# Kernel tuning notes

Hardware: AMD Instinct MI355X
Metric: run time of the kernel (lower is better)

## Reference

```python
import jax, jax.numpy as jnp
import numpy as np

B, L, DIM = 2, 2048, 2048
N_HEADS, N_KV_HEADS = 32, 8
HEAD_DIM = DIM // N_HEADS  # 64
SCALE = HEAD_DIM ** -0.5


def setup_inputs() -> dict:
    key = jax.random.key(0)
    ks = jax.random.split(key, 6)
    s = 0.02
    x = jax.random.normal(ks[0], (B, L, DIM), dtype=jnp.float32)
    wq = jax.random.normal(ks[1], (N_HEADS * HEAD_DIM, DIM), dtype=jnp.float32) * s
    wk = jax.random.normal(ks[2], (N_KV_HEADS * HEAD_DIM, DIM), dtype=jnp.float32) * s
    wv = jax.random.normal(ks[3], (N_KV_HEADS * HEAD_DIM, DIM), dtype=jnp.float32) * s
    wo = jax.random.normal(ks[4], (DIM, N_HEADS * HEAD_DIM), dtype=jnp.float32) * s
    # standard RoPE frequencies: theta = 10000^(-2i/d), angle = pos * theta
    inv_freq = 1.0 / (10000.0 ** (jnp.arange(0, HEAD_DIM, 2, dtype=jnp.float32) / HEAD_DIM))
    angles = jnp.arange(L, dtype=jnp.float32)[:, None] * inv_freq[None, :]  # [L, HEAD_DIM//2]
    freqs_cos = jnp.cos(angles)
    freqs_sin = jnp.sin(angles)
    # additive causal mask [1, 1, L, L]
    causal = jnp.tril(jnp.ones((L, L), dtype=bool))
    mask = jnp.where(causal, 0.0, -1e9).astype(jnp.float32)[None, None]
    return {"x": x, "wq": wq, "wk": wk, "wv": wv, "wo": wo,
            "freqs_cos": freqs_cos, "freqs_sin": freqs_sin, "mask": mask}


def _apply_rope(t, cos, sin):
    # t: [B, H, L, D]; complex pairing is (even, odd) interleaved along D
    te, to = t[..., 0::2], t[..., 1::2]
    cos = cos[None, None, : t.shape[2], :]
    sin = sin[None, None, : t.shape[2], :]
    re = te * cos - to * sin
    im = te * sin + to * cos
    return jnp.stack([re, im], axis=-1).reshape(t.shape)


def reference(x, wq, wk, wv, wo, freqs_cos, freqs_sin, mask):
    b, l, _ = x.shape
    q = (x @ wq.T).reshape(b, l, N_HEADS, HEAD_DIM).transpose(0, 2, 1, 3)
    k = (x @ wk.T).reshape(b, l, N_KV_HEADS, HEAD_DIM).transpose(0, 2, 1, 3)
    v = (x @ wv.T).reshape(b, l, N_KV_HEADS, HEAD_DIM).transpose(0, 2, 1, 3)
    q = _apply_rope(q, freqs_cos, freqs_sin)
    k = _apply_rope(k, freqs_cos, freqs_sin)
    repeats = N_HEADS // N_KV_HEADS
    k = jnp.repeat(k, repeats, axis=1)
    v = jnp.repeat(v, repeats, axis=1)
    scores = jnp.einsum("bhqd,bhkd->bhqk", q, k) * SCALE + mask
    probs = jax.nn.softmax(scores, axis=-1)
    out = jnp.einsum("bhqk,bhkd->bhqd", probs, v)
    out = out.transpose(0, 2, 1, 3).reshape(b, l, N_HEADS * HEAD_DIM)
    return out @ wo.T
```

## Files before the change

### kernel.cpp

```cpp
#include <hip/hip_runtime.h>
#include <hip/hip_bf16.h>
#include <stdint.h>

typedef __attribute__((ext_vector_type(8))) short bf16x8;
typedef __attribute__((ext_vector_type(4))) float f32x4;
typedef __attribute__((ext_vector_type(16))) float f32x16;
typedef __attribute__((ext_vector_type(4))) unsigned int u32x4;

#define B_    2
#define L_    2048
#define DIM_  2048
#define NH_   32
#define NKV_  8
#define HD_   64
#define KVD_  512
#define CLOG_ 0.1803368801111244f

__device__ __forceinline__ unsigned short f2bf(float f) {
  unsigned u = __float_as_uint(f);
  u += 0x7fff + ((u >> 16) & 1);
  return (unsigned short)(u >> 16);
}
__device__ __forceinline__ unsigned cvtpk(float lo, float hi_) {
  unsigned r;
  asm("v_cvt_pk_bf16_f32 %0, %1, %2" : "=v"(r) : "v"(lo), "v"(hi_));
  return r;
}
__device__ __forceinline__ float bf2f(unsigned short h) {
  return __uint_as_float(((unsigned)h) << 16);
}

#define GLDS16(gsrc, ldst) __builtin_amdgcn_global_load_lds( \
    (const __attribute__((address_space(1))) unsigned int*)(gsrc), \
    (__attribute__((address_space(3))) unsigned int*)(ldst), 16, 0, 0)

__global__ void cvt_all(const float* __restrict__ x,  const float* __restrict__ wq,
                        const float* __restrict__ wk, const float* __restrict__ wv,
                        const float* __restrict__ wo,
                        unsigned short* __restrict__ xb,  unsigned short* __restrict__ wqb,
                        unsigned short* __restrict__ wkb, unsigned short* __restrict__ wvb,
                        unsigned short* __restrict__ wob) {
  int i = blockIdx.x * blockDim.x + threadIdx.x;
  const float* src; unsigned short* dst; int off;
  if (i < 2097152)      { src = x;  dst = xb;  off = i; }
  else if (i < 3145728) { src = wq; dst = wqb; off = i - 2097152; }
  else if (i < 3407872) { src = wk; dst = wkb; off = i - 3145728; }
  else if (i < 3670016) { src = wv; dst = wvb; off = i - 3407872; }
  else                  { src = wo; dst = wob; off = i - 3670016; }
  float4 v = reinterpret_cast<const float4*>(src)[off];
  ushort4 o;
  o.x = f2bf(v.x); o.y = f2bf(v.y); o.z = f2bf(v.z); o.w = f2bf(v.w);
  reinterpret_cast<ushort4*>(dst)[off] = o;
}

template<int OUTMODE>
__device__ __forceinline__ void gemm128_core(
    const unsigned short* __restrict__ A,
    const unsigned short* __restrict__ W,
    void* __restrict__ C, int N, int K, int m0, int n0,
    unsigned short (*As)[128 * 64], unsigned short (*Bs)[128 * 64])
{
  const int tid = threadIdx.x;
  const int lane = tid & 63, wid = tid >> 6;
  const int wm = wid >> 1, wn = wid & 1;
  const int r = lane & 15, g = lane >> 4;
  const int rsw = (r & 7) << 4;
  f32x4 acc[4][4] = {};

  auto STAGE = [&](int buf, int k0) {
#pragma unroll
    for (int p = 0; p < 4; ++p) {
      int off = (p * 256 + tid) * 16;
      int row = off >> 7;
      int colb = (off & 127) ^ ((row & 7) << 4);
      GLDS16((const char*)A + ((size_t)(m0 + row) * K + k0) * 2 + colb,
             (char*)As[buf] + off);
      GLDS16((const char*)W + ((size_t)(n0 + row) * K + k0) * 2 + colb,
             (char*)Bs[buf] + off);
    }
  };

  const int nt = K >> 6;
  STAGE(0, 0);
  asm volatile("s_waitcnt vmcnt(0)" ::: "memory");
  __builtin_amdgcn_s_barrier();
  int cur = 0;
  for (int kt = 0; kt < nt; ++kt) {
    if (kt + 1 < nt) {
      STAGE(cur ^ 1, (kt + 1) << 6);
      asm volatile("s_waitcnt vmcnt(8)" ::: "memory");
    } else {
      asm volatile("s_waitcnt vmcnt(0)" ::: "memory");
    }
    __builtin_amdgcn_s_barrier();
    __builtin_amdgcn_sched_barrier(0);
    const char* Ab = (const char*)As[cur];
    const char* Bb = (const char*)Bs[cur];
    __builtin_amdgcn_s_setprio(1);
#pragma unroll
    for (int kk = 0; kk < 2; ++kk) {
      bf16x8 af[4], bfv[4];
#pragma unroll
      for (int i = 0; i < 4; ++i)
        af[i] = *reinterpret_cast<const bf16x8*>(
            Ab + (wm * 64 + i * 16 + r) * 128 + ((kk * 64 + g * 16) ^ rsw));
#pragma unroll
      for (int i = 0; i < 4; ++i)
        bfv[i] = *reinterpret_cast<const bf16x8*>(
            Bb + (wn * 64 + i * 16 + r) * 128 + ((kk * 64 + g * 16) ^ rsw));
#pragma unroll
      for (int i = 0; i < 4; ++i)
#pragma unroll
        for (int j = 0; j < 4; ++j)
          acc[i][j] = __builtin_amdgcn_mfma_f32_16x16x32_bf16(af[i], bfv[j], acc[i][j], 0, 0, 0);
    }
    __builtin_amdgcn_s_setprio(0);
    asm volatile("s_waitcnt lgkmcnt(0)" ::: "memory");
    __builtin_amdgcn_s_barrier();
    cur ^= 1;
  }

  if (OUTMODE == 2) {
#pragma unroll
    for (int i = 0; i < 4; ++i)
#pragma unroll
      for (int jf = 0; jf < 4; ++jf) {
        int col = n0 + wn * 64 + jf * 16 + r;
        int kvi = col >> 6, d = col & 63;
        int tok = m0 + wm * 64 + i * 16 + g * 4;
        int bb = tok >> 11, tl = tok & (L_ - 1);
        uint2 u;
        u.x = cvtpk(acc[i][jf][0], acc[i][jf][1]);
        u.y = cvtpk(acc[i][jf][2], acc[i][jf][3]);
        *reinterpret_cast<uint2*>((unsigned short*)C +
            ((size_t)((bb * NKV_ + kvi) * HD_ + d)) * L_ + tl) = u;
      }
  } else {
#pragma unroll
    for (int i = 0; i < 4; ++i)
#pragma unroll
      for (int jf = 0; jf < 4; ++jf)
#pragma unroll
        for (int j = 0; j < 4; ++j) {
          size_t row = (size_t)(m0 + wm * 64 + i * 16 + g * 4 + j);
          size_t col = (size_t)(n0 + wn * 64 + jf * 16 + r);
          float v = acc[i][jf][j];
          if (OUTMODE == 1) ((float*)C)[row * N + col] = v;
          else ((unsigned short*)C)[row * N + col] = f2bf(v);
        }
  }
}

template<int OUT_F32>
__global__ __launch_bounds__(256) void gemm_bt(
    const unsigned short* __restrict__ A,
    const unsigned short* __restrict__ W,
    void* __restrict__ C, int M, int N, int K)
{
  __shared__ unsigned short As[2][128 * 64];
  __shared__ unsigned short Bs[2][128 * 64];
  gemm128_core<OUT_F32 ? 1 : 0>(A, W, C, N, K, blockIdx.y * 128, blockIdx.x * 128, As, Bs);
}

__global__ __launch_bounds__(256) void gemm_qkv(
    const unsigned short* __restrict__ A,
    const unsigned short* __restrict__ Wq,
    const unsigned short* __restrict__ Wk,
    const unsigned short* __restrict__ Wv,
    unsigned short* __restrict__ Cq,
    unsigned short* __restrict__ Ck,
    unsigned short* __restrict__ Vt)
{
  __shared__ unsigned short As[2][128 * 64];
  __shared__ unsigned short Bs[2][128 * 64];
  const int bx = blockIdx.x;
  const int m0 = blockIdx.y * 128;
  if (bx < 16)
    gemm128_core<0>(A, Wq, Cq, 2048, DIM_, m0, bx * 128, As, Bs);
  else if (bx < 20)
    gemm128_core<0>(A, Wk, Ck, 512, DIM_, m0, (bx - 16) * 128, As, Bs);
  else
    gemm128_core<2>(A, Wv, Vt, 512, DIM_, m0, (bx - 20) * 128, As, Bs);
}

__global__ void rope_v8(unsigned short* __restrict__ t,
                        const float* __restrict__ fc,
                        const float* __restrict__ fs,
                        int rowElems, int lshift, float scale) {
  int idx = blockIdx.x * blockDim.x + threadIdx.x;
  int row = idx >> lshift;
  if (row >= B_ * L_) return;
  int pos = (idx & ((1 << lshift) - 1)) << 3;
  int l = row & (L_ - 1);
  int i0 = (pos & 63) >> 1;
  unsigned short* p = t + (size_t)row * rowElems + pos;
  uint4 v = *reinterpret_cast<const uint4*>(p);
  float4 c4 = *reinterpret_cast<const float4*>(fc + l * 32 + i0);
  float4 s4 = *reinterpret_cast<const float4*>(fs + l * 32 + i0);
  float cc[4] = {c4.x * scale, c4.y * scale, c4.z * scale, c4.w * scale};
  float ss[4] = {s4.x * scale, s4.y * scale, s4.z * scale, s4.w * scale};
  unsigned wds[4] = {v.x, v.y, v.z, v.w};
  uint4 o;
  unsigned ow[4];
#pragma unroll
  for (int k = 0; k < 4; ++k) {
    float te = bf2f((unsigned short)(wds[k] & 0xffff));
    float to = bf2f((unsigned short)(wds[k] >> 16));
    ow[k] = cvtpk(te * cc[k] - to * ss[k], te * ss[k] + to * cc[k]);
  }
  o.x = ow[0]; o.y = ow[1]; o.z = ow[2]; o.w = ow[3];
  *reinterpret_cast<uint4*>(p) = o;
}

__global__ __launch_bounds__(256) void attn_kernel(
    const unsigned short* __restrict__ Q,
    const unsigned short* __restrict__ K,
    const unsigned short* __restrict__ Vt,
    unsigned short* __restrict__ AO)
{
  __shared__ unsigned short Ks[2][64 * 64];
  __shared__ unsigned short Vs[2][64 * 64];
  const int tid = threadIdx.x;
  const int lane = tid & 63, w = tid >> 6;
  const int ql = lane & 31;
  const int hi = lane >> 5;
  const int wid = blockIdx.x;
  const int j = wid >> 6;
  const int blk = j >> 2, pos = j & 3;
  const int base = 15 - 4 * blk;
  const int qt = (blk & 1) ? (base - 3 + pos) : (base - pos);
  const int bh = wid & 63;
  const int b = bh >> 5, h = bh & 31, kv = h >> 2;
  const int q0 = qt * 128;
  const int qw = q0 + w * 32;
  const int nkt = (q0 + 128) >> 6;

  bf16x8 qf[4];
  const unsigned short* qbase = Q + ((size_t)(b * L_ + qw + ql)) * DIM_ + h * HD_ + hi * 8;
#pragma unroll
  for (int dk = 0; dk < 4; ++dk)
    qf[dk] = *reinterpret_cast<const bf16x8*>(qbase + dk * 16);

  const unsigned short* Kg = K + (size_t)b * L_ * KVD_ + kv * HD_;
  const unsigned short* Vg = Vt + ((size_t)(b * NKV_ + kv)) * HD_ * L_;

  f32x16 oacc0 = {}, oacc1 = {};
  float lrow = 0.f;
  const int rsw = (ql & 7) << 4;

  auto STAGE = [&](int buf, int t) {
    const int k0 = t * 64;
#pragma unroll
    for (int p = 0; p < 2; ++p) {
      int off = (p * 256 + tid) * 16;
      int row = off >> 7;
      int colb = (off & 127) ^ ((row & 7) << 4);
      GLDS16((const char*)Kg + ((size_t)(k0 + row)) * (KVD_ * 2) + colb,
             (char*)Ks[buf] + off);
      GLDS16((const char*)Vg + ((size_t)row) * (L_ * 2) + (size_t)k0 * 2 + colb,
             (char*)Vs[buf] + off);
    }
  };

  int cur = 0;
  STAGE(0, 0);
  __syncthreads();

  for (int t = 0; t < nkt; ++t) {
    if (t + 1 < nkt) STAGE(cur ^ 1, t + 1);
    const int k0 = t * 64;
    if (k0 < qw + 32) {
      const char* Kl = (const char*)Ks[cur];
      const char* Vl = (const char*)Vs[cur];
      f32x16 s0 = {}, s1 = {};
      __builtin_amdgcn_s_setprio(1);
#pragma unroll
      for (int dk = 0; dk < 4; ++dk) {
        bf16x8 kf0 = *reinterpret_cast<const bf16x8*>(Kl + ql * 128 + ((dk * 32 + hi * 16) ^ rsw));
        bf16x8 kf1 = *reinterpret_cast<const bf16x8*>(Kl + (32 + ql) * 128 + ((dk * 32 + hi * 16) ^ rsw));
        s0 = __builtin_amdgcn_mfma_f32_32x32x16_bf16(kf0, qf[dk], s0, 0, 0, 0);
        s1 = __builtin_amdgcn_mfma_f32_32x32x16_bf16(kf1, qf[dk], s1, 0, 0, 0);
      }
      __builtin_amdgcn_s_setprio(0);
      float p[32];
      float ps = 0.f;
      if (k0 + 63 > qw) {
        int q = qw + ql;
#pragma unroll
        for (int i = 0; i < 32; ++i) {
          float sv = (i < 16) ? s0[i] : s1[i - 16];
          int kk = k0 + (i >> 4) * 32 + (i & 3) + 8 * ((i & 15) >> 2) + 4 * hi;
          float e = exp2f(sv);
          e = (kk > q) ? 0.f : e;
          p[i] = e; ps += e;
        }
      } else {
#pragma unroll
        for (int i = 0; i < 32; ++i) {
          float sv = (i < 16) ? s0[i] : s1[i - 16];
          p[i] = exp2f(sv); ps += p[i];
        }
      }
      ps += __shfl_xor(ps, 32);
      lrow += ps;
      bf16x8 pf[4];
#pragma unroll
      for (int s = 0; s < 4; ++s) {
        int bp = ((s >> 1) << 4) + ((s & 1) << 3);
        unsigned w0 = cvtpk(p[bp + 0], p[bp + 1]);
        unsigned w1 = cvtpk(p[bp + 2], p[bp + 3]);
        unsigned w2 = cvtpk(p[bp + 4], p[bp + 5]);
        unsigned w3 = cvtpk(p[bp + 6], p[bp + 7]);
        unsigned x0 = (unsigned)__shfl_xor((int)w0, 32);
        unsigned x1 = (unsigned)__shfl_xor((int)w1, 32);
        unsigned x2 = (unsigned)__shfl_xor((int)w2, 32);
        unsigned x3 = (unsigned)__shfl_xor((int)w3, 32);
        u32x4 fw;
        fw[0] = hi ? x2 : w0;
        fw[1] = hi ? x3 : w1;
        fw[2] = hi ? w2 : x0;
        fw[3] = hi ? w3 : x1;
        pf[s] = __builtin_bit_cast(bf16x8, fw);
      }
      __builtin_amdgcn_s_setprio(1);
#pragma unroll
      for (int s = 0; s < 4; ++s) {
        bf16x8 v0 = *reinterpret_cast<const bf16x8*>(Vl + ql * 128 + ((s * 32 + hi * 16) ^ rsw));
        bf16x8 v1 = *reinterpret_cast<const bf16x8*>(Vl + (32 + ql) * 128 + ((s * 32 + hi * 16) ^ rsw));
        oacc0 = __builtin_amdgcn_mfma_f32_32x32x16_bf16(v0, pf[s], oacc0, 0, 0, 0);
        oacc1 = __builtin_amdgcn_mfma_f32_32x32x16_bf16(v1, pf[s], oacc1, 0, 0, 0);
      }
      __builtin_amdgcn_s_setprio(0);
    }
    __syncthreads();
    cur ^= 1;
  }

  float inv = 1.f / lrow;
  unsigned short* obase = AO + ((size_t)(b * L_ + qw + ql)) * DIM_ + h * HD_;
#pragma unroll
  for (int g4 = 0; g4 < 4; ++g4) {
    uint2 u;
    u.x = cvtpk(oacc0[g4 * 4 + 0] * inv, oacc0[g4 * 4 + 1] * inv);
    u.y = cvtpk(oacc0[g4 * 4 + 2] * inv, oacc0[g4 * 4 + 3] * inv);
    *reinterpret_cast<uint2*>(obase + g4 * 8 + hi * 4) = u;
    uint2 v;
    v.x = cvtpk(oacc1[g4 * 4 + 0] * inv, oacc1[g4 * 4 + 1] * inv);
    v.y = cvtpk(oacc1[g4 * 4 + 2] * inv, oacc1[g4 * 4 + 3] * inv);
    *reinterpret_cast<uint2*>(obase + 32 + g4 * 8 + hi * 4) = v;
  }
}

extern "C" void kernel_launch(void* const* d_in, const int* in_sizes, int n_in,
                              void* d_out, int out_size, void* d_ws, size_t ws_size,
                              hipStream_t stream) {
  const float* x  = (const float*)d_in[0];
  const float* wq = (const float*)d_in[1];
  const float* wk = (const float*)d_in[2];
  const float* wv = (const float*)d_in[3];
  const float* wo = (const float*)d_in[4];
  const float* fc = (const float*)d_in[5];
  const float* fs = (const float*)d_in[6];
  float* out = (float*)d_out;

  unsigned short* ws  = (unsigned short*)d_ws;
  unsigned short* xb  = ws;
  unsigned short* wqb = xb  + 8388608;
  unsigned short* wkb = wqb + 4194304;
  unsigned short* wvb = wkb + 1048576;
  unsigned short* wob = wvb + 1048576;
  unsigned short* Qb  = wob + 4194304;
  unsigned short* Kb  = Qb  + 8388608;
  unsigned short* Vtb = Kb  + 2097152;
  unsigned short* AOb = Vtb + 2097152;

  cvt_all<<<18432, 256, 0, stream>>>(x, wq, wk, wv, wo, xb, wqb, wkb, wvb, wob);

  gemm_qkv<<<dim3(24, 32), 256, 0, stream>>>(xb, wqb, wkb, wvb, Qb, Kb, Vtb);

  rope_v8<<<4096, 256, 0, stream>>>(Qb, fc, fs, 2048, 8, CLOG_);
  rope_v8<<<1024, 256, 0, stream>>>(Kb, fc, fs, 512, 6, 1.0f);

  attn_kernel<<<1024, 256, 0, stream>>>(Qb, Kb, Vtb, AOb);

  gemm_bt<1><<<dim3(16, 32), 256, 0, stream>>>(AOb, wob, out, 4096, 2048, 2048);
}
```

Measured before the change: 226.5 us.

## Use permlane32 swap for P fragments and split-wait barriers in attention loop

```diff
diff --git a/kernel.cpp b/kernel.cpp
--- a/kernel.cpp
+++ b/kernel.cpp
@@ -28,6 +28,17 @@
 }
 __device__ __forceinline__ float bf2f(unsigned short h) {
   return __uint_as_float(((unsigned)h) << 16);
+}
+__device__ __forceinline__ void plswap2(unsigned &a, unsigned &b, int hi) {
+#if __has_builtin(__builtin_amdgcn_permlane32_swap)
+  auto r = __builtin_amdgcn_permlane32_swap(a, b, false, false);
+  a = (unsigned)r[0]; b = (unsigned)r[1];
+#else
+  unsigned xa = (unsigned)__shfl_xor((int)a, 32);
+  unsigned xb = (unsigned)__shfl_xor((int)b, 32);
+  unsigned na = hi ? xb : a, nb = hi ? b : xa;
+  a = na; b = nb;
+#endif
 }
 
 #define GLDS16(gsrc, ldst) __builtin_amdgcn_global_load_lds( \
@@ -264,10 +275,18 @@
 
   int cur = 0;
   STAGE(0, 0);
-  __syncthreads();
+  asm volatile("s_waitcnt vmcnt(0)" ::: "memory");
+  __builtin_amdgcn_s_barrier();
 
   for (int t = 0; t < nkt; ++t) {
-    if (t + 1 < nkt) STAGE(cur ^ 1, t + 1);
+    if (t + 1 < nkt) {
+      STAGE(cur ^ 1, t + 1);
+      asm volatile("s_waitcnt vmcnt(4)" ::: "memory");
+    } else {
+      asm volatile("s_waitcnt vmcnt(0)" ::: "memory");
+    }
+    __builtin_amdgcn_s_barrier();
+    __builtin_amdgcn_sched_barrier(0);
     const int k0 = t * 64;
     if (k0 < qw + 32) {
       const char* Kl = (const char*)Ks[cur];
@@ -301,7 +320,6 @@
           p[i] = exp2f(sv); ps += p[i];
         }
       }
-      ps += __shfl_xor(ps, 32);
       lrow += ps;
       bf16x8 pf[4];
 #pragma unroll
@@ -311,15 +329,10 @@
         unsigned w1 = cvtpk(p[bp + 2], p[bp + 3]);
         unsigned w2 = cvtpk(p[bp + 4], p[bp + 5]);
         unsigned w3 = cvtpk(p[bp + 6], p[bp + 7]);
-        unsigned x0 = (unsigned)__shfl_xor((int)w0, 32);
-        unsigned x1 = (unsigned)__shfl_xor((int)w1, 32);
-        unsigned x2 = (unsigned)__shfl_xor((int)w2, 32);
-        unsigned x3 = (unsigned)__shfl_xor((int)w3, 32);
+        plswap2(w0, w2, hi);
+        plswap2(w1, w3, hi);
         u32x4 fw;
-        fw[0] = hi ? x2 : w0;
-        fw[1] = hi ? x3 : w1;
-        fw[2] = hi ? w2 : x0;
-        fw[3] = hi ? w3 : x1;
+        fw[0] = w0; fw[1] = w1; fw[2] = w2; fw[3] = w3;
         pf[s] = __builtin_bit_cast(bf16x8, fw);
       }
       __builtin_amdgcn_s_setprio(1);
@@ -332,11 +345,15 @@
       }
       __builtin_amdgcn_s_setprio(0);
     }
-    __syncthreads();
+    asm volatile("s_waitcnt lgkmcnt(0)" ::: "memory");
+    __builtin_amdgcn_s_barrier();
     cur ^= 1;
   }
 
-  float inv = 1.f / lrow;
+  unsigned la = __float_as_uint(lrow), lb = __float_as_uint(lrow);
+  plswap2(la, lb, hi);
+  float ltot = __uint_as_float(la) + __uint_as_float(lb);
+  float inv = 1.f / ltot;
   unsigned short* obase = AO + ((size_t)(b * L_ + qw + ql)) * DIM_ + h * HD_;
 #pragma unroll
   for (int g4 = 0; g4 < 4; ++g4) {
```

Measured after the change: 221.3 us. 1.02x faster.
